# Kernel optimization log

Measured on AMD Instinct MI355X. Metric: run time of the kernel, lower is better.

## Reference

```python
import jax, jax.numpy as jnp
import numpy as np
from jax import lax

INPUT_SCALE = 1.0
RES_SCALE = 1.0


def setup_inputs() -> dict:
    key = jax.random.key(0)
    k1, k2, k3, k4 = jax.random.split(key, 4)
    seq_len, input_size, res_size = 4096, 512, 2048
    return {
        "input_data": jax.random.normal(k1, (seq_len, input_size), dtype=jnp.float32),
        "initial_state": jax.random.normal(k2, (res_size,), dtype=jnp.float32),
        "W_in": jax.random.normal(k3, (res_size, input_size), dtype=jnp.float32),
        "W_res": jax.random.normal(k4, (res_size, res_size), dtype=jnp.float32),
    }


def reference(input_data, initial_state, W_in, W_res):
    # state_t = tanh(input_scale * W_in @ x_t + res_scale * W_res @ state_{t-1}) / sqrt(res_size)
    res_size = W_res.shape[0]
    inv_sqrt = jnp.asarray(1.0 / np.sqrt(res_size), dtype=input_data.dtype)
    # Precompute input projection for all timesteps as one GEMM: (seq_len, res_size)
    pre = (INPUT_SCALE * input_data) @ W_in.T

    def step(state, u_t):
        new_state = jnp.tanh(u_t + RES_SCALE * (W_res @ state)) * inv_sqrt
        return new_state, new_state

    _, states = lax.scan(step, initial_state, pre)
    # (seq_len + 1, res_size): row 0 is the initial state
    return jnp.concatenate([initial_state[None, :], states], axis=0)
```

## Files before the change

### kernel.cpp

```cpp
#include <hip/hip_runtime.h>

constexpr int SEQ  = 4096;
constexpr int IN   = 512;
constexpr int RS   = 2048;
constexpr int GB   = 64;
constexpr int BT   = 1024;
constexpr int RING = 8;
constexpr float INV_SQRT = 0.022097086912079612f;

__global__ __launch_bounds__(256)
void gemm_pre_kernel(const float* __restrict__ A, const float* __restrict__ B,
                     float* __restrict__ out) {
    __shared__ float As[64][17];
    __shared__ float Bs[64][17];
    const int tid = threadIdx.x;
    const int tx = tid & 15, ty = tid >> 4;
    const int m0 = blockIdx.x * 64, n0 = blockIdx.y * 64;
    const int lr = tid >> 2;
    const int lk = (tid & 3) * 4;
    float acc[4][4] = {};
    for (int k0 = 0; k0 < IN; k0 += 16) {
        const float4 av = *(const float4*)&A[(size_t)(m0 + lr) * IN + k0 + lk];
        const float4 bv = *(const float4*)&B[(size_t)(n0 + lr) * IN + k0 + lk];
        __syncthreads();
        As[lr][lk + 0] = av.x; As[lr][lk + 1] = av.y;
        As[lr][lk + 2] = av.z; As[lr][lk + 3] = av.w;
        Bs[lr][lk + 0] = bv.x; Bs[lr][lk + 1] = bv.y;
        Bs[lr][lk + 2] = bv.z; Bs[lr][lk + 3] = bv.w;
        __syncthreads();
#pragma unroll
        for (int k = 0; k < 16; ++k) {
            float a[4], b[4];
#pragma unroll
            for (int i = 0; i < 4; ++i) a[i] = As[ty * 4 + i][k];
#pragma unroll
            for (int j = 0; j < 4; ++j) b[j] = Bs[tx * 4 + j][k];
#pragma unroll
            for (int i = 0; i < 4; ++i)
#pragma unroll
                for (int j = 0; j < 4; ++j) acc[i][j] += a[i] * b[j];
        }
    }
#pragma unroll
    for (int i = 0; i < 4; ++i) {
        float4 v = make_float4(acc[i][0], acc[i][1], acc[i][2], acc[i][3]);
        *(float4*)&out[(size_t)(m0 + ty * 4 + i + 1) * RS + n0 + tx * 4] = v;
    }
}

__device__ __forceinline__ float fast_tanh(float x) {
    float e = __expf(2.0f * x);
    return 1.0f - 2.0f * __builtin_amdgcn_rcpf(e + 1.0f);
}

typedef unsigned long long u64;
#define AT_LOAD_U64(p)     __hip_atomic_load((p), __ATOMIC_RELAXED, __HIP_MEMORY_SCOPE_AGENT)
#define AT_STORE_U32(p, v) __hip_atomic_store((p), (v), __ATOMIC_RELAXED, __HIP_MEMORY_SCOPE_AGENT)

__global__ __launch_bounds__(BT, 1)
void reservoir_scan_kernel(const float* __restrict__ W_res,
                           const float* __restrict__ init,
                           float* __restrict__ out,
                           unsigned* __restrict__ ring32) {
    __shared__ float s_state[RS];
    __shared__ float s_pub[32];
    u64* ring = (u64*)ring32;
    const int bid  = blockIdx.x;
    const int tid  = threadIdx.x;
    const int wave = tid >> 6;
    const int lane = tid & 63;
    const int r0   = bid * 32 + wave * 2;

    const float* wp0 = W_res + (size_t)r0 * RS + lane * 4;
    const float* wp1 = wp0 + RS;
    float4 w0[8], w1[8];
#pragma unroll
    for (int j = 0; j < 8; ++j) {
        w0[j] = *(const float4*)(wp0 + j * 256);
        w1[j] = *(const float4*)(wp1 + j * 256);
    }
#pragma unroll
    for (int j = 0; j < 8; ++j) {
        asm volatile("" : "+v"(w0[j].x), "+v"(w0[j].y), "+v"(w0[j].z), "+v"(w0[j].w));
        asm volatile("" : "+v"(w1[j].x), "+v"(w1[j].y), "+v"(w1[j].z), "+v"(w1[j].w));
    }

    if (wave == 0 && lane < 32) {
        float v = init[bid * 32 + lane];
        out[bid * 32 + lane] = v;
        s_pub[lane] = v;
        AT_STORE_U32(ring32 + bid * 32 + lane, __float_as_uint(v) | 1u);
    }
    __syncthreads();

    for (int t = 0; t < SEQ; ++t) {
        const size_t crow = (size_t)(t & (RING - 1)) * (RS / 2);
        const size_t prow = (size_t)((t + 1) & (RING - 1)) * RS;
        const unsigned tag_c = ((unsigned)(t >> 3) & 1u) ^ 1u;
        const unsigned tag_p = ((unsigned)((t + 1) >> 3) & 1u) ^ 1u;

        float pre = 0.f;
        if (lane < 2) pre = out[(size_t)(t + 1) * RS + r0 + lane];

        if ((tid >> 4) == bid) {
            const int k = tid & 15;
            s_state[2 * tid]     = s_pub[2 * k];
            s_state[2 * tid + 1] = s_pub[2 * k + 1];
        } else {
            const u64* pp = ring + crow + tid;
            u64 v = AT_LOAD_U64(pp);
            while (((((unsigned)v ^ tag_c) & 1u) |
                    (((unsigned)(v >> 32) ^ tag_c) & 1u)) != 0u)
                v = AT_LOAD_U64(pp);
            s_state[2 * tid]     = __uint_as_float((unsigned)v);
            s_state[2 * tid + 1] = __uint_as_float((unsigned)(v >> 32));
        }
        __syncthreads();

        float a0 = 0.f, a1 = 0.f;
#pragma unroll
        for (int j = 0; j < 8; ++j) {
            const float4 sv = *(const float4*)&s_state[lane * 4 + j * 256];
            a0 += w0[j].x * sv.x + w0[j].y * sv.y + w0[j].z * sv.z + w0[j].w * sv.w;
            a1 += w1[j].x * sv.x + w1[j].y * sv.y + w1[j].z * sv.z + w1[j].w * sv.w;
        }
#pragma unroll
        for (int off = 32; off > 0; off >>= 1) {
            a0 += __shfl_xor(a0, off);
            a1 += __shfl_xor(a1, off);
        }

        if (lane < 2) {
            float a = lane ? a1 : a0;
            float s = fast_tanh(pre + a) * INV_SQRT;
            out[(size_t)(t + 1) * RS + r0 + lane] = s;
            s_pub[wave * 2 + lane] = s;
        }
        __syncthreads();

        if (wave == 0 && lane < 32) {
            unsigned bits = __float_as_uint(s_pub[lane]);
            AT_STORE_U32(ring32 + prow + bid * 32 + lane,
                         (bits & ~1u) | tag_p);
        }
    }
}

extern "C" void kernel_launch(void* const* d_in, const int* in_sizes, int n_in,
                              void* d_out, int out_size, void* d_ws, size_t ws_size,
                              hipStream_t stream) {
    const float* x     = (const float*)d_in[0];
    const float* init  = (const float*)d_in[1];
    const float* W_in  = (const float*)d_in[2];
    const float* W_res = (const float*)d_in[3];
    float* out = (float*)d_out;
    unsigned* ring = (unsigned*)d_ws;

    hipMemsetAsync(d_ws, 0, (size_t)RING * RS * sizeof(float), stream);
    gemm_pre_kernel<<<dim3(SEQ / 64, RS / 64), 256, 0, stream>>>(x, W_in, out);

    void* args[] = { (void*)&W_res, (void*)&init, (void*)&out, (void*)&ring };
    hipLaunchCooperativeKernel((void*)reservoir_scan_kernel,
                               dim3(GB), dim3(BT), args, 0, stream);
}
```

Measured before the change: 8.159 ms.

## Halve scan block size, four rows per wave with butterfly transpose-reduce

The persistent scan kernel now runs 512-thread blocks where each wave holds four W_res rows in registers instead of two, keeping the same grid and rows per block. Each thread polls two ring entries and writes a float4 into shared state. The cross-lane reduction becomes a transpose-style butterfly, so the four row sums take fewer shuffles than four independent reductions. The aim is to cut per-step barrier and shuffle cost and widen state loads, at the price of twice the register footprint per thread and fewer waves to hide latency.

```diff
diff --git a/kernel.cpp b/kernel.cpp
--- a/kernel.cpp
+++ b/kernel.cpp
@@ -4,7 +4,7 @@
 constexpr int IN   = 512;
 constexpr int RS   = 2048;
 constexpr int GB   = 64;
-constexpr int BT   = 1024;
+constexpr int BT   = 512;
 constexpr int RING = 8;
 constexpr float INV_SQRT = 0.022097086912079612f;
 
@@ -57,7 +57,7 @@
 #define AT_LOAD_U64(p)     __hip_atomic_load((p), __ATOMIC_RELAXED, __HIP_MEMORY_SCOPE_AGENT)
 #define AT_STORE_U32(p, v) __hip_atomic_store((p), (v), __ATOMIC_RELAXED, __HIP_MEMORY_SCOPE_AGENT)
 
-__global__ __launch_bounds__(BT, 1)
+__global__ __launch_bounds__(BT, 2)
 void reservoir_scan_kernel(const float* __restrict__ W_res,
                            const float* __restrict__ init,
                            float* __restrict__ out,
@@ -69,21 +69,21 @@
     const int tid  = threadIdx.x;
     const int wave = tid >> 6;
     const int lane = tid & 63;
-    const int r0   = bid * 32 + wave * 2;
+    const int r0   = bid * 32 + wave * 4;
 
-    const float* wp0 = W_res + (size_t)r0 * RS + lane * 4;
-    const float* wp1 = wp0 + RS;
-    float4 w0[8], w1[8];
+    float4 w[4][8];
 #pragma unroll
-    for (int j = 0; j < 8; ++j) {
-        w0[j] = *(const float4*)(wp0 + j * 256);
-        w1[j] = *(const float4*)(wp1 + j * 256);
+    for (int r = 0; r < 4; ++r) {
+        const float* wp = W_res + (size_t)(r0 + r) * RS + lane * 4;
+#pragma unroll
+        for (int j = 0; j < 8; ++j) w[r][j] = *(const float4*)(wp + j * 256);
     }
 #pragma unroll
-    for (int j = 0; j < 8; ++j) {
-        asm volatile("" : "+v"(w0[j].x), "+v"(w0[j].y), "+v"(w0[j].z), "+v"(w0[j].w));
-        asm volatile("" : "+v"(w1[j].x), "+v"(w1[j].y), "+v"(w1[j].z), "+v"(w1[j].w));
-    }
+    for (int r = 0; r < 4; ++r)
+#pragma unroll
+        for (int j = 0; j < 8; ++j)
+            asm volatile("" : "+v"(w[r][j].x), "+v"(w[r][j].y),
+                              "+v"(w[r][j].z), "+v"(w[r][j].w));
 
     if (wave == 0 && lane < 32) {
         float v = init[bid * 32 + lane];
@@ -100,41 +100,57 @@
         const unsigned tag_p = ((unsigned)((t + 1) >> 3) & 1u) ^ 1u;
 
         float pre = 0.f;
-        if (lane < 2) pre = out[(size_t)(t + 1) * RS + r0 + lane];
+        if (lane < 4) pre = out[(size_t)(t + 1) * RS + r0 + lane];
 
-        if ((tid >> 4) == bid) {
-            const int k = tid & 15;
-            s_state[2 * tid]     = s_pub[2 * k];
-            s_state[2 * tid + 1] = s_pub[2 * k + 1];
+        if ((tid >> 3) == bid) {
+            const int k = tid & 7;
+            *(float4*)&s_state[4 * tid] = *(const float4*)&s_pub[4 * k];
         } else {
-            const u64* pp = ring + crow + tid;
-            u64 v = AT_LOAD_U64(pp);
-            while (((((unsigned)v ^ tag_c) & 1u) |
-                    (((unsigned)(v >> 32) ^ tag_c) & 1u)) != 0u)
-                v = AT_LOAD_U64(pp);
-            s_state[2 * tid]     = __uint_as_float((unsigned)v);
-            s_state[2 * tid + 1] = __uint_as_float((unsigned)(v >> 32));
+            const u64* pp = ring + crow + 2 * tid;
+            u64 v0 = AT_LOAD_U64(pp);
+            u64 v1 = AT_LOAD_U64(pp + 1);
+#define RDY(x) (((((unsigned)(x) ^ tag_c) | ((unsigned)((x) >> 32) ^ tag_c)) & 1u) == 0u)
+            while (!(RDY(v0) && RDY(v1))) {
+                v0 = AT_LOAD_U64(pp);
+                v1 = AT_LOAD_U64(pp + 1);
+            }
+#undef RDY
+            float4 sv;
+            sv.x = __uint_as_float((unsigned)v0);
+            sv.y = __uint_as_float((unsigned)(v0 >> 32));
+            sv.z = __uint_as_float((unsigned)v1);
+            sv.w = __uint_as_float((unsigned)(v1 >> 32));
+            *(float4*)&s_state[4 * tid] = sv;
         }
         __syncthreads();
 
-        float a0 = 0.f, a1 = 0.f;
+        float a0 = 0.f, a1 = 0.f, a2 = 0.f, a3 = 0.f;
 #pragma unroll
         for (int j = 0; j < 8; ++j) {
             const float4 sv = *(const float4*)&s_state[lane * 4 + j * 256];
-            a0 += w0[j].x * sv.x + w0[j].y * sv.y + w0[j].z * sv.z + w0[j].w * sv.w;
-            a1 += w1[j].x * sv.x + w1[j].y * sv.y + w1[j].z * sv.z + w1[j].w * sv.w;
-        }
-#pragma unroll
-        for (int off = 32; off > 0; off >>= 1) {
-            a0 += __shfl_xor(a0, off);
-            a1 += __shfl_xor(a1, off);
+            a0 += w[0][j].x * sv.x + w[0][j].y * sv.y + w[0][j].z * sv.z + w[0][j].w * sv.w;
+            a1 += w[1][j].x * sv.x + w[1][j].y * sv.y + w[1][j].z * sv.z + w[1][j].w * sv.w;
+            a2 += w[2][j].x * sv.x + w[2][j].y * sv.y + w[2][j].z * sv.z + w[2][j].w * sv.w;
+            a3 += w[3][j].x * sv.x + w[3][j].y * sv.y + w[3][j].z * sv.z + w[3][j].w * sv.w;
         }
 
-        if (lane < 2) {
-            float a = lane ? a1 : a0;
-            float s = fast_tanh(pre + a) * INV_SQRT;
+        const bool p1 = (lane & 1) != 0;
+        float k01 = p1 ? a1 : a0, s01 = p1 ? a0 : a1;
+        k01 += __shfl_xor(s01, 1);
+        float k23 = p1 ? a3 : a2, s23 = p1 ? a2 : a3;
+        k23 += __shfl_xor(s23, 1);
+        const bool p2 = (lane & 2) != 0;
+        float kk = p2 ? k23 : k01, ss = p2 ? k01 : k23;
+        kk += __shfl_xor(ss, 2);
+        kk += __shfl_xor(kk, 4);
+        kk += __shfl_xor(kk, 8);
+        kk += __shfl_xor(kk, 16);
+        kk += __shfl_xor(kk, 32);
+
+        if (lane < 4) {
+            float s = fast_tanh(pre + kk) * INV_SQRT;
             out[(size_t)(t + 1) * RS + r0 + lane] = s;
-            s_pub[wave * 2 + lane] = s;
+            s_pub[wave * 4 + lane] = s;
         }
         __syncthreads();
 
```

Result: faster. 7.793 ms (-4.5%).
